# Performance work log

Hardware: AMD Instinct MI355X
Metric: run time of the kernel (lower is better)

## Reference

```python
import jax, jax.numpy as jnp
import numpy as np

N_NODES = 100000
N_GRAPHS = 64


def gcn_conv(x, src, dst, W, b, num_nodes):
    """PyG GCNConv: add self-loops, symmetric deg normalization, aggregate at dst."""
    h = x @ W  # [N, out]
    ones_e = jnp.ones(src.shape[0], dtype=x.dtype)
    # degree includes self-loop (+1)
    deg = jax.ops.segment_sum(ones_e, dst, num_segments=num_nodes) + 1.0
    dinv = jnp.where(deg > 0, 1.0 / jnp.sqrt(deg), 0.0)  # deg>=1 always here
    norm = dinv[src] * dinv[dst]  # [E]
    msg = h[src] * norm[:, None]  # gather + scale
    agg = jax.ops.segment_sum(msg, dst, num_segments=num_nodes)
    # self-loop contribution: norm_ii = dinv[i]^2
    agg = agg + h * (dinv * dinv)[:, None]
    return agg + b


def global_mean_pool(x, batch, num_graphs):
    sums = jax.ops.segment_sum(x, batch, num_segments=num_graphs)
    counts = jax.ops.segment_sum(jnp.ones(x.shape[0], dtype=x.dtype), batch,
                                 num_segments=num_graphs)
    return sums / jnp.maximum(counts, 1.0)[:, None]


def setup_inputs() -> dict:
    key = jax.random.key(0)
    ks = jax.random.split(key, 8)
    H = 128
    x = jax.random.normal(ks[0], (N_NODES, 4), dtype=jnp.float32)
    edge_index = jax.random.randint(ks[1], (2, 1600000), 0, N_NODES, dtype=jnp.int64 if jax.config.read('jax_enable_x64') else jnp.int32)
    batch = jnp.sort(jax.random.randint(ks[2], (N_NODES,), 0, N_GRAPHS))
    def glorot(k, shape):
        fan_in, fan_out = shape
        lim = np.sqrt(6.0 / (fan_in + fan_out))
        return jax.random.uniform(k, shape, jnp.float32, -lim, lim)
    return {
        'x': x,
        'edge_index': edge_index,
        'batch': batch,
        'W1': glorot(ks[3], (4, H)), 'b1': jnp.zeros((H,), jnp.float32),
        'W2': glorot(ks[4], (H, H)), 'b2': jnp.zeros((H,), jnp.float32),
        'W3': glorot(ks[5], (H, H)), 'b3': jnp.zeros((H,), jnp.float32),
        'Wl': glorot(ks[6], (H, 2)), 'bl': jnp.zeros((2,), jnp.float32),
    }


def reference(x, edge_index, batch, W1, b1, W2, b2, W3, b3, Wl, bl):
    src, dst = edge_index[0], edge_index[1]
    h = jax.nn.relu(gcn_conv(x, src, dst, W1, b1, N_NODES))
    h = jax.nn.relu(gcn_conv(h, src, dst, W2, b2, N_NODES))
    h = jax.nn.relu(gcn_conv(h, src, dst, W3, b3, N_NODES))
    g = global_mean_pool(h, batch, N_GRAPHS)  # [G, H]
    logits = g @ Wl + bl  # [G, 2]
    return jax.nn.log_softmax(logits, axis=1)
```

## Files before the change

### kernel.cpp

```cpp
#include <hip/hip_runtime.h>

#define HDIM 128
#define NGRAPH 64

#define BSHIFT 9
#define NBUCK 196
#define BCAP 48
#define BSTR 49
#define RCAP 9216
#define BIN_CHUNK 4096

typedef __attribute__((ext_vector_type(8))) short short8;
typedef __attribute__((ext_vector_type(4))) float floatx4;
typedef __attribute__((ext_vector_type(2))) float floatx2;

__device__ __forceinline__ float bf2f(unsigned short u) {
    union { unsigned int i; float f; } v;
    v.i = ((unsigned int)u) << 16;
    return v.f;
}
__device__ __forceinline__ unsigned short f2bf(float f) {
    unsigned int u = __float_as_uint(f);
    u += 0x7FFFu + ((u >> 16) & 1u);
    return (unsigned short)(u >> 16);
}

__global__ __launch_bounds__(256) void k_misc(int* __restrict__ gcur,
                                              const int* __restrict__ batch,
                                              float* __restrict__ gcnt,
                                              float* __restrict__ gsum,
                                              const float* __restrict__ W2,
                                              unsigned short* __restrict__ Wp2,
                                              const float* __restrict__ W3,
                                              unsigned short* __restrict__ Wp3,
                                              int N, int nbuck) {
    int t = threadIdx.x;
    int blk = blockIdx.x;
    if (blk == 0) {
        if (t < nbuck) gcur[t] = t * RCAP;
        for (int i = t; i < NGRAPH * 128; i += 256) gsum[i] = 0.f;
        if (t < NGRAPH) {
            int g = t;
            int lo = 0, hi = N;
            while (lo < hi) { int m = (lo + hi) >> 1; if (batch[m] < g) lo = m + 1; else hi = m; }
            int lb = lo;
            lo = 0; hi = N;
            while (lo < hi) { int m = (lo + hi) >> 1; if (batch[m] < g + 1) lo = m + 1; else hi = m; }
            gcnt[g] = (float)(lo - lb);
        }
        return;
    }
    const float* W = (blk <= 64) ? W2 : W3;
    unsigned short* Wp = (blk <= 64) ? Wp2 : Wp3;
    int idx = ((blk <= 64) ? (blk - 1) : (blk - 65)) * 256 + t;
    int j = idx & 7, l = (idx >> 3) & 63, frag = idx >> 9;
    int c = frag >> 2, ks = frag & 3;
    int k = ks * 32 + ((l >> 4) & 3) * 8 + j;
    int n = c * 16 + (l & 15);
    Wp[idx] = f2bf(W[k * 128 + n]);
}


__global__ __launch_bounds__(256) void k_binA(const int* __restrict__ src,
                                              const int* __restrict__ dst,
                                              int* __restrict__ gcur,
                                              unsigned int* __restrict__ binned, int E) {
    __shared__ unsigned int bin[NBUCK * BSTR];
    __shared__ int bcnt[NBUCK];
    __shared__ int bbase[NBUCK];
    int t = threadIdx.x;
    for (int b = t; b < NBUCK; b += 256) bcnt[b] = 0;
    __syncthreads();
    int e0 = blockIdx.x * BIN_CHUNK;
    #pragma unroll
    for (int i = 0; i < BIN_CHUNK / 1024; i++) {
        int e = e0 + i * 1024 + t * 4;
        if (e + 3 < E) {
            const int4 d4 = *(const int4*)&dst[e];
            const int4 s4 = *(const int4*)&src[e];
            int dd[4] = {d4.x, d4.y, d4.z, d4.w};
            int ss[4] = {s4.x, s4.y, s4.z, s4.w};
            #pragma unroll
            for (int k = 0; k < 4; k++) {
                int d = dd[k];
                unsigned int rec = ((unsigned int)(d & 511) << 20) | (unsigned int)ss[k];
                int b = d >> BSHIFT;
                int idx = atomicAdd(&bcnt[b], 1);
                if (idx < BCAP) bin[b * BSTR + idx] = rec;
                else { int p = atomicAdd(&gcur[b], 1); binned[p] = rec; }
            }
        } else {
            for (int k = 0; k < 4; k++) {
                int e2 = e + k;
                if (e2 < E) {
                    int d = dst[e2];
                    unsigned int rec = ((unsigned int)(d & 511) << 20) | (unsigned int)src[e2];
                    int b = d >> BSHIFT;
                    int idx = atomicAdd(&bcnt[b], 1);
                    if (idx < BCAP) bin[b * BSTR + idx] = rec;
                    else { int p = atomicAdd(&gcur[b], 1); binned[p] = rec; }
                }
            }
        }
    }
    __syncthreads();
    if (t < NBUCK) {
        int cnt = min(bcnt[t], BCAP);
        bbase[t] = atomicAdd(&gcur[t], cnt);
    }
    __syncthreads();
    int wave = t >> 6, lane = t & 63;
    for (int b = wave; b < NBUCK; b += 4) {
        int cnt = min(bcnt[b], BCAP);
        int base = bbase[b];
        if (lane < cnt) binned[base + lane] = bin[b * BSTR + lane];
    }
}

__global__ __launch_bounds__(256) void k_fillB(const int* __restrict__ gcur,
                                               const unsigned int* __restrict__ binned,
                                               int* __restrict__ P,
                                               float* __restrict__ dinv,
                                               int* __restrict__ csr, int N, int nbuck) {
    __shared__ int ps[256];
    __shared__ int cnt[512];
    __shared__ int image[RCAP];
    int b = blockIdx.x;
    int t = threadIdx.x;
    int lt = (t < nbuck) ? (gcur[t] - t * RCAP) : 0;
    ps[t] = lt;
    __syncthreads();
    for (int d = 1; d < 256; d <<= 1) {
        int o = (t >= d) ? ps[t - d] : 0;
        __syncthreads();
        ps[t] += o;
        __syncthreads();
    }
    int start = (b > 0) ? ps[b - 1] : 0;
    int len = ps[b] - start;
    __syncthreads();

    int n0 = b << BSHIFT;
    int nloc = min(n0 + 512, N) - n0;
    cnt[t] = 0; cnt[t + 256] = 0;
    __syncthreads();
    const unsigned int* rb = binned + (size_t)b * RCAP;
    for (int i = t; i < len; i += 256) atomicAdd(&cnt[rb[i] >> 20], 1);
    __syncthreads();
    int c0 = cnt[2 * t], c1 = cnt[2 * t + 1];
    int pair = c0 + c1;
    __syncthreads();
    cnt[t] = pair;
    __syncthreads();
    for (int d = 1; d < 256; d <<= 1) {
        int o = (t >= d) ? cnt[t - d] : 0;
        __syncthreads();
        cnt[t] += o;
        __syncthreads();
    }
    int excl = cnt[t] - pair;
    __syncthreads();
    if (2 * t < nloc) {
        P[n0 + 2 * t] = start + excl;
        dinv[n0 + 2 * t] = rsqrtf((float)c0 + 1.0f);
    }
    if (2 * t + 1 < nloc) {
        P[n0 + 2 * t + 1] = start + excl + c0;
        dinv[n0 + 2 * t + 1] = rsqrtf((float)c1 + 1.0f);
    }
    if (b == nbuck - 1 && t == 0) P[N] = start + len;
    cnt[2 * t] = excl;
    cnt[2 * t + 1] = excl + c0;
    __syncthreads();
    for (int i = t; i < len; i += 256) {
        unsigned int rec = rb[i];
        int pos = atomicAdd(&cnt[rec >> 20], 1);
        image[pos] = (int)(rec & 0xFFFFFu);
    }
    __syncthreads();
    for (int i = t; i < len; i += 256) csr[start + i] = image[i];
}

__global__ void k_xscale(const float4* __restrict__ x, const float* __restrict__ dinv,
                         float4* __restrict__ xs, int N) {
    int n = blockIdx.x * blockDim.x + threadIdx.x;
    if (n < N) {
        float dd = dinv[n];
        float4 v = x[n];
        xs[n] = make_float4(v.x * dd, v.y * dd, v.z * dd, v.w * dd);
    }
}

__global__ void k_aggx_csr(const int* __restrict__ P, const int* __restrict__ csr,
                           const float4* __restrict__ xs, const float* __restrict__ dinv,
                           float4* __restrict__ aggx, int N) {
    int d = blockIdx.x * blockDim.x + threadIdx.x;
    if (d >= N) return;
    int s0 = P[d], s1 = P[d + 1];
    float dd = dinv[d];
    float4 sv = xs[d];
    float4 a = make_float4(sv.x * dd, sv.y * dd, sv.z * dd, sv.w * dd);
    int i = s0;
    int pre = min(s1, (s0 + 3) & ~3);
    for (; i < pre; i++) {
        float4 v = xs[csr[i]];
        a.x += v.x; a.y += v.y; a.z += v.z; a.w += v.w;
    }
    for (; i + 8 <= s1; i += 8) {
        const int4 iA = *(const int4*)&csr[i];
        const int4 iB = *(const int4*)&csr[i + 4];
        float4 vA = xs[iA.x], vB = xs[iA.y], vC = xs[iA.z], vD = xs[iA.w];
        float4 vE = xs[iB.x], vF = xs[iB.y], vG = xs[iB.z], vH = xs[iB.w];
        a.x += vA.x + vB.x + vC.x + vD.x + vE.x + vF.x + vG.x + vH.x;
        a.y += vA.y + vB.y + vC.y + vD.y + vE.y + vF.y + vG.y + vH.y;
        a.z += vA.z + vB.z + vC.z + vD.z + vE.z + vF.z + vG.z + vH.z;
        a.w += vA.w + vB.w + vC.w + vD.w + vE.w + vF.w + vG.w + vH.w;
    }
    for (; i + 4 <= s1; i += 4) {
        const int4 ix = *(const int4*)&csr[i];
        float4 vA = xs[ix.x], vB = xs[ix.y], vC = xs[ix.z], vD = xs[ix.w];
        a.x += vA.x + vB.x + vC.x + vD.x;
        a.y += vA.y + vB.y + vC.y + vD.y;
        a.z += vA.z + vB.z + vC.z + vD.z;
        a.w += vA.w + vB.w + vC.w + vD.w;
    }
    for (; i < s1; i++) {
        float4 v = xs[csr[i]];
        a.x += v.x; a.y += v.y; a.z += v.z; a.w += v.w;
    }
    aggx[d] = make_float4(a.x * dd, a.y * dd, a.z * dd, a.w * dd);
}

#define LXS 136
__global__ __launch_bounds__(256) void k_l1t2(const float4* __restrict__ aggx,
                                              const float* __restrict__ W1,
                                              const float* __restrict__ b1,
                                              const unsigned short* __restrict__ Wp,
                                              const float* __restrict__ dinv,
                                              unsigned char* __restrict__ out8, int N) {
    __shared__ unsigned short lx[64 * LXS];
    __shared__ unsigned short lw[16384];
    __shared__ float w1s[512];
    __shared__ float b1s[128];
    __shared__ float ax[64][4];
    int t = threadIdx.x;
    int n0 = blockIdx.x * 64;

    for (int i = t; i < 512; i += 256) w1s[i] = W1[i];
    if (t < 128) b1s[t] = b1[t];
    if (t < 64) {
        float4 v = (n0 + t < N) ? aggx[n0 + t] : make_float4(0.f, 0.f, 0.f, 0.f);
        ax[t][0] = v.x; ax[t][1] = v.y; ax[t][2] = v.z; ax[t][3] = v.w;
    }
    for (int ch = t; ch < 2048; ch += 256)
        *(uint4*)&lw[ch * 8] = *(const uint4*)&Wp[ch * 8];
    __syncthreads();

    for (int i = t; i < 8192; i += 256) {
        int n = i >> 7, j = i & 127;
        float v = b1s[j] + ax[n][0] * w1s[j] + ax[n][1] * w1s[128 + j]
                         + ax[n][2] * w1s[256 + j] + ax[n][3] * w1s[384 + j];
        lx[n * LXS + j] = f2bf(fmaxf(v, 0.f));
    }
    __syncthreads();

    int w = t >> 6, lane = t & 63;
    int m0 = w * 16;
    int col = lane & 15, quad = lane >> 4;

    short8 afrag[4];
    #pragma unroll
    for (int ks = 0; ks < 4; ks++)
        afrag[ks] = *(const short8*)&lx[(m0 + col) * LXS + ks * 32 + quad * 8];

    float dv[4];
    #pragma unroll
    for (int r = 0; r < 4; r++) {
        int gn = n0 + m0 + quad * 4 + r;
        dv[r] = (gn < N) ? dinv[gn] : 0.0f;
    }

    #pragma unroll
    for (int c = 0; c < 8; c++) {
        floatx4 acc = {0.f, 0.f, 0.f, 0.f};
        #pragma unroll
        for (int ks = 0; ks < 4; ks++) {
            const short8 bfrag = *(const short8*)&lw[((c * 4 + ks) * 64 + lane) * 8];
            acc = __builtin_amdgcn_mfma_f32_16x16x32_bf16(afrag[ks], bfrag, acc, 0, 0, 0);
        }
        #pragma unroll
        for (int r = 0; r < 4; r++) {
            int gn = n0 + m0 + quad * 4 + r;
            if (gn < N) {
                float v = acc[r] * dv[r];
                out8[(size_t)gn * 128 + c * 16 + col] =
                    (unsigned char)(__builtin_amdgcn_cvt_pk_fp8_f32(v, v, 0, false) & 0xFF);
            }
        }
    }
}

__global__ __launch_bounds__(256) void k_transform_mfma(const unsigned short* __restrict__ in,
                                                        const unsigned short* __restrict__ Wp,
                                                        const float* __restrict__ dinv,
                                                        unsigned char* __restrict__ out8, int N) {
    __shared__ unsigned short lx[64 * LXS];
    __shared__ unsigned short lw[16384];
    int t = threadIdx.x;
    int n0 = blockIdx.x * 64;

    for (int ch = t; ch < 1024; ch += 256) {
        int row = ch >> 4, part = ch & 15;
        uint4 val = make_uint4(0, 0, 0, 0);
        if (n0 + row < N) val = *(const uint4*)&in[(size_t)(n0 + row) * 128 + part * 8];
        *(uint4*)&lx[row * LXS + part * 8] = val;
    }
    for (int ch = t; ch < 2048; ch += 256)
        *(uint4*)&lw[ch * 8] = *(const uint4*)&Wp[ch * 8];
    __syncthreads();

    int w = t >> 6, lane = t & 63;
    int m0 = w * 16;
    int col = lane & 15, quad = lane >> 4;

    short8 afrag[4];
    #pragma unroll
    for (int ks = 0; ks < 4; ks++)
        afrag[ks] = *(const short8*)&lx[(m0 + col) * LXS + ks * 32 + quad * 8];

    float dv[4];
    #pragma unroll
    for (int r = 0; r < 4; r++) {
        int gn = n0 + m0 + quad * 4 + r;
        dv[r] = (gn < N) ? dinv[gn] : 0.0f;
    }

    #pragma unroll
    for (int c = 0; c < 8; c++) {
        floatx4 acc = {0.f, 0.f, 0.f, 0.f};
        #pragma unroll
        for (int ks = 0; ks < 4; ks++) {
            const short8 bfrag = *(const short8*)&lw[((c * 4 + ks) * 64 + lane) * 8];
            acc = __builtin_amdgcn_mfma_f32_16x16x32_bf16(afrag[ks], bfrag, acc, 0, 0, 0);
        }
        #pragma unroll
        for (int r = 0; r < 4; r++) {
            int gn = n0 + m0 + quad * 4 + r;
            if (gn < N) {
                float v = acc[r] * dv[r];
                out8[(size_t)gn * 128 + c * 16 + col] =
                    (unsigned char)(__builtin_amdgcn_cvt_pk_fp8_f32(v, v, 0, false) & 0xFF);
            }
        }
    }
}

__device__ __forceinline__ void fp8acc(unsigned int u, float& a0, float& a1,
                                       float& a2, float& a3) {
    floatx2 lo = __builtin_amdgcn_cvt_pk_f32_fp8(u, false);
    floatx2 hi = __builtin_amdgcn_cvt_pk_f32_fp8(u, true);
    a0 += lo.x; a1 += lo.y; a2 += hi.x; a3 += hi.y;
}

__device__ __forceinline__ void gather_fp8(const int* __restrict__ csr,
                                           const unsigned int* __restrict__ hs8,
                                           int s0, int s1, int lane,
                                           float& a0, float& a1, float& a2, float& a3) {
    int i = s0;
    int pre = min(s1, (s0 + 3) & ~3);
    for (; i < pre; i++)
        fp8acc(hs8[(size_t)csr[i] * 32 + lane], a0, a1, a2, a3);
    for (; i + 8 <= s1; i += 8) {
        const int4 iA = *(const int4*)&csr[i];
        const int4 iB = *(const int4*)&csr[i + 4];
        unsigned int u0 = hs8[(size_t)iA.x * 32 + lane];
        unsigned int u1 = hs8[(size_t)iA.y * 32 + lane];
        unsigned int u2 = hs8[(size_t)iA.z * 32 + lane];
        unsigned int u3 = hs8[(size_t)iA.w * 32 + lane];
        unsigned int u4 = hs8[(size_t)iB.x * 32 + lane];
        unsigned int u5 = hs8[(size_t)iB.y * 32 + lane];
        unsigned int u6 = hs8[(size_t)iB.z * 32 + lane];
        unsigned int u7 = hs8[(size_t)iB.w * 32 + lane];
        fp8acc(u0, a0, a1, a2, a3); fp8acc(u1, a0, a1, a2, a3);
        fp8acc(u2, a0, a1, a2, a3); fp8acc(u3, a0, a1, a2, a3);
        fp8acc(u4, a0, a1, a2, a3); fp8acc(u5, a0, a1, a2, a3);
        fp8acc(u6, a0, a1, a2, a3); fp8acc(u7, a0, a1, a2, a3);
    }
    for (; i + 4 <= s1; i += 4) {
        const int4 iA = *(const int4*)&csr[i];
        unsigned int u0 = hs8[(size_t)iA.x * 32 + lane];
        unsigned int u1 = hs8[(size_t)iA.y * 32 + lane];
        unsigned int u2 = hs8[(size_t)iA.z * 32 + lane];
        unsigned int u3 = hs8[(size_t)iA.w * 32 + lane];
        fp8acc(u0, a0, a1, a2, a3); fp8acc(u1, a0, a1, a2, a3);
        fp8acc(u2, a0, a1, a2, a3); fp8acc(u3, a0, a1, a2, a3);
    }
    for (; i < s1; i++)
        fp8acc(hs8[(size_t)csr[i] * 32 + lane], a0, a1, a2, a3);
}

__global__ __launch_bounds__(256) void k_agg_csr(const int* __restrict__ P,
                                                 const int* __restrict__ csr,
                                                 const unsigned int* __restrict__ hs8,
                                                 const float* __restrict__ dinv,
                                                 const float* __restrict__ bias,
                                                 unsigned short* __restrict__ out16,
                                                 unsigned int* __restrict__ out8,
                                                 int N, int write8) {
    int g = (blockIdx.x * 256 + threadIdx.x) >> 5;
    int lane = threadIdx.x & 31;
    if (g >= N) return;
    int s0 = P[g], s1 = P[g + 1];
    unsigned int su = hs8[(size_t)g * 32 + lane];
    floatx2 slo = __builtin_amdgcn_cvt_pk_f32_fp8(su, false);
    floatx2 shi = __builtin_amdgcn_cvt_pk_f32_fp8(su, true);
    float a0 = slo.x, a1 = slo.y, a2 = shi.x, a3 = shi.y;
    gather_fp8(csr, hs8, s0, s1, lane, a0, a1, a2, a3);
    float dd = dinv[g];
    const float4 bb = *(const float4*)&bias[lane * 4];
    float o0 = fmaxf(a0 * dd + bb.x, 0.f);
    float o1 = fmaxf(a1 * dd + bb.y, 0.f);
    float o2 = fmaxf(a2 * dd + bb.z, 0.f);
    float o3 = fmaxf(a3 * dd + bb.w, 0.f);
    if (write8) {
        unsigned int wv = __builtin_amdgcn_cvt_pk_fp8_f32(o0, o1, 0, false);
        wv = __builtin_amdgcn_cvt_pk_fp8_f32(o2, o3, wv, true);
        out8[(size_t)g * 32 + lane] = wv;
    } else {
        ushort4 o;
        o.x = f2bf(o0); o.y = f2bf(o1); o.z = f2bf(o2); o.w = f2bf(o3);
        *(ushort4*)&out16[(size_t)g * 128 + lane * 4] = o;
    }
}

#define POOL_ROWS 64
__global__ __launch_bounds__(128) void k_pool8(const unsigned char* __restrict__ h8,
                                               const int* __restrict__ batch,
                                               float* __restrict__ gsum, int N) {
    int n0 = blockIdx.x * POOL_ROWS;
    if (n0 >= N) return;
    int len = min(POOL_ROWS, N - n0);
    int j = threadIdx.x;
    int bFirst = batch[n0];
    int bLast = batch[n0 + len - 1];
    if (bFirst == bLast) {
        float acc = 0.f;
        #pragma unroll 8
        for (int i = 0; i < len; i++) {
            unsigned int u = h8[(size_t)(n0 + i) * 128 + j];
            floatx2 lo = __builtin_amdgcn_cvt_pk_f32_fp8(u, false);
            acc += lo.x;
        }
        unsafeAtomicAdd(&gsum[(size_t)bFirst * 128 + j], acc);
    } else {
        float acc = 0.f;
        int cur = bFirst;
        for (int i = 0; i < len; i++) {
            int b = batch[n0 + i];
            if (b != cur) {
                unsafeAtomicAdd(&gsum[(size_t)cur * 128 + j], acc);
                acc = 0.f; cur = b;
            }
            unsigned int u = h8[(size_t)(n0 + i) * 128 + j];
            floatx2 lo = __builtin_amdgcn_cvt_pk_f32_fp8(u, false);
            acc += lo.x;
        }
        unsafeAtomicAdd(&gsum[(size_t)cur * 128 + j], acc);
    }
}

__global__ __launch_bounds__(256) void k_head(const float* __restrict__ gsum,
                                              const float* __restrict__ gcnt,
                                              const float* __restrict__ Wl,
                                              const float* __restrict__ bl,
                                              float* __restrict__ out, int G) {
    int t = threadIdx.x;
    int g = t >> 2, q = t & 3;
    if (g >= G) return;
    float l0 = 0.f, l1 = 0.f;
    #pragma unroll
    for (int k = 0; k < 32; k++) {
        int jj = q * 32 + k;
        float v = gsum[(size_t)g * 128 + jj];
        l0 += v * Wl[jj * 2 + 0];
        l1 += v * Wl[jj * 2 + 1];
    }
    l0 += __shfl_xor(l0, 1, 64); l1 += __shfl_xor(l1, 1, 64);
    l0 += __shfl_xor(l0, 2, 64); l1 += __shfl_xor(l1, 2, 64);
    if (q == 0) {
        float inv = 1.0f / fmaxf(gcnt[g], 1.0f);
        l0 = l0 * inv + bl[0];
        l1 = l1 * inv + bl[1];
        float m = fmaxf(l0, l1);
        float lse = m + logf(expf(l0 - m) + expf(l1 - m));
        out[g * 2 + 0] = l0 - lse;
        out[g * 2 + 1] = l1 - lse;
    }
}


extern "C" void kernel_launch(void* const* d_in, const int* in_sizes, int n_in,
                              void* d_out, int out_size, void* d_ws, size_t ws_size,
                              hipStream_t stream) {
    const float* x   = (const float*)d_in[0];
    const int*   ei  = (const int*)d_in[1];
    const int*   bat = (const int*)d_in[2];
    const float* W1  = (const float*)d_in[3];
    const float* b1  = (const float*)d_in[4];
    const float* W2  = (const float*)d_in[5];
    const float* b2  = (const float*)d_in[6];
    const float* W3  = (const float*)d_in[7];
    const float* b3  = (const float*)d_in[8];
    const float* Wl  = (const float*)d_in[9];
    const float* bl  = (const float*)d_in[10];

    const int N = in_sizes[0] / 4;
    const int E = in_sizes[1] / 2;
    const int* srcI = ei;
    const int* dstI = ei + E;

    const int nbuck = (N + 511) >> BSHIFT;
    const int pAlloc = ((N + 1 + 3) & ~3) + 4;

    float* wsf  = (float*)d_ws;
    float* dinv = wsf;
    int*   P    = (int*)(dinv + N);
    int*   csr  = P + pAlloc;
    float* aggx = (float*)(csr + E);
    unsigned short* bufA16 = (unsigned short*)(aggx + (size_t)N * 4);
    unsigned char*  hs8    = (unsigned char*)(bufA16 + (size_t)N * 128);
    unsigned short* Wp2    = (unsigned short*)(hs8 + (size_t)N * 128);
    unsigned short* Wp3    = Wp2 + 16384;
    float* gsum = (float*)(Wp3 + 16384);
    float* gcnt = gsum + NGRAPH * 128;
    int*   gcur = (int*)(gcnt + NGRAPH);
    unsigned int* binned = (unsigned int*)hs8;
    float* xs4 = (float*)bufA16;
    unsigned char* h3f8  = (unsigned char*)bufA16;

    k_misc<<<129, 256, 0, stream>>>(gcur, bat, gcnt, gsum, W2, Wp2, W3, Wp3, N, nbuck);
    k_binA<<<(E + BIN_CHUNK - 1) / BIN_CHUNK, 256, 0, stream>>>(srcI, dstI, gcur, binned, E);
    k_fillB<<<nbuck, 256, 0, stream>>>(gcur, binned, P, dinv, csr, N, nbuck);

    k_xscale<<<(N + 255) / 256, 256, 0, stream>>>((const float4*)x, dinv, (float4*)xs4, N);
    k_aggx_csr<<<(N + 255) / 256, 256, 0, stream>>>(P, csr, (const float4*)xs4, dinv,
                                                    (float4*)aggx, N);
    k_l1t2<<<(N + 63) / 64, 256, 0, stream>>>((const float4*)aggx, W1, b1, Wp2, dinv, hs8, N);

    k_agg_csr<<<(N * 32 + 255) / 256, 256, 0, stream>>>(P, csr, (const unsigned int*)hs8,
                                                        dinv, b2, bufA16, nullptr, N, 0);

    k_transform_mfma<<<(N + 63) / 64, 256, 0, stream>>>(bufA16, Wp3, dinv, hs8, N);
    k_agg_csr<<<(N * 32 + 255) / 256, 256, 0, stream>>>(P, csr, (const unsigned int*)hs8,
                                                        dinv, b3, nullptr,
                                                        (unsigned int*)h3f8, N, 1);

    k_pool8<<<(N + POOL_ROWS - 1) / POOL_ROWS, 128, 0, stream>>>(h3f8, bat, gsum, N);
    k_head<<<1, 256, 0, stream>>>(gsum, gcnt, Wl, bl, (float*)d_out, NGRAPH);
}
```

Baseline: 320.9 us.

## Fuse x scaling into CSR fill, split edge gather per node, fuse pooling

Folds the dinv scaling of x into k_fillB and drops the separate k_xscale launch. Aggregation now gives each node a full 64-lane wave, with two 32-lane halves each gathering half the edge range and combining through a cross-half shuffle. The final-layer aggregation writes its ReLU output straight into per-graph sums through shared memory and atomics, which removes the fp8 intermediate store and the k_pool8 pass. The cost is twice as many threads per node, half of them idle in the epilogue, plus a block-wide sync in the pooling path. Pooling now uses full fp32 outputs instead of fp8-rounded ones.

New measurement: 375.7 us. +17.1%, slower.

```diff
diff --git a/kernel.cpp b/kernel.cpp
--- a/kernel.cpp
+++ b/kernel.cpp
@@ -121,7 +121,10 @@
                                                const unsigned int* __restrict__ binned,
                                                int* __restrict__ P,
                                                float* __restrict__ dinv,
-                                               int* __restrict__ csr, int N, int nbuck) {
+                                               int* __restrict__ csr,
+                                               const float4* __restrict__ x4,
+                                               float4* __restrict__ xs4,
+                                               int N, int nbuck) {
     __shared__ int ps[256];
     __shared__ int cnt[512];
     __shared__ int image[RCAP];
@@ -161,12 +164,20 @@
     int excl = cnt[t] - pair;
     __syncthreads();
     if (2 * t < nloc) {
-        P[n0 + 2 * t] = start + excl;
-        dinv[n0 + 2 * t] = rsqrtf((float)c0 + 1.0f);
+        int n = n0 + 2 * t;
+        float dv0 = rsqrtf((float)c0 + 1.0f);
+        P[n] = start + excl;
+        dinv[n] = dv0;
+        float4 xv = x4[n];
+        xs4[n] = make_float4(xv.x * dv0, xv.y * dv0, xv.z * dv0, xv.w * dv0);
     }
     if (2 * t + 1 < nloc) {
-        P[n0 + 2 * t + 1] = start + excl + c0;
-        dinv[n0 + 2 * t + 1] = rsqrtf((float)c1 + 1.0f);
+        int n = n0 + 2 * t + 1;
+        float dv1 = rsqrtf((float)c1 + 1.0f);
+        P[n] = start + excl + c0;
+        dinv[n] = dv1;
+        float4 xv = x4[n];
+        xs4[n] = make_float4(xv.x * dv1, xv.y * dv1, xv.z * dv1, xv.w * dv1);
     }
     if (b == nbuck - 1 && t == 0) P[N] = start + len;
     cnt[2 * t] = excl;
@@ -179,16 +190,6 @@
     }
     __syncthreads();
     for (int i = t; i < len; i += 256) csr[start + i] = image[i];
-}
-
-__global__ void k_xscale(const float4* __restrict__ x, const float* __restrict__ dinv,
-                         float4* __restrict__ xs, int N) {
-    int n = blockIdx.x * blockDim.x + threadIdx.x;
-    if (n < N) {
-        float dd = dinv[n];
-        float4 v = x[n];
-        xs[n] = make_float4(v.x * dd, v.y * dd, v.z * dd, v.w * dd);
-    }
 }
 
 __global__ void k_aggx_csr(const int* __restrict__ P, const int* __restrict__ csr,
@@ -405,67 +406,68 @@
                                                  const float* __restrict__ dinv,
                                                  const float* __restrict__ bias,
                                                  unsigned short* __restrict__ out16,
-                                                 unsigned int* __restrict__ out8,
-                                                 int N, int write8) {
-    int g = (blockIdx.x * 256 + threadIdx.x) >> 5;
-    int lane = threadIdx.x & 31;
-    if (g >= N) return;
-    int s0 = P[g], s1 = P[g + 1];
-    unsigned int su = hs8[(size_t)g * 32 + lane];
-    floatx2 slo = __builtin_amdgcn_cvt_pk_f32_fp8(su, false);
-    floatx2 shi = __builtin_amdgcn_cvt_pk_f32_fp8(su, true);
-    float a0 = slo.x, a1 = slo.y, a2 = shi.x, a3 = shi.y;
-    gather_fp8(csr, hs8, s0, s1, lane, a0, a1, a2, a3);
-    float dd = dinv[g];
-    const float4 bb = *(const float4*)&bias[lane * 4];
-    float o0 = fmaxf(a0 * dd + bb.x, 0.f);
-    float o1 = fmaxf(a1 * dd + bb.y, 0.f);
-    float o2 = fmaxf(a2 * dd + bb.z, 0.f);
-    float o3 = fmaxf(a3 * dd + bb.w, 0.f);
-    if (write8) {
-        unsigned int wv = __builtin_amdgcn_cvt_pk_fp8_f32(o0, o1, 0, false);
-        wv = __builtin_amdgcn_cvt_pk_fp8_f32(o2, o3, wv, true);
-        out8[(size_t)g * 32 + lane] = wv;
+                                                 const int* __restrict__ batch,
+                                                 float* __restrict__ gsum,
+                                                 int N, int mode) {
+    __shared__ float psum[4][128];
+    int wv = threadIdx.x >> 6;
+    int g = blockIdx.x * 4 + wv;
+    int lane = threadIdx.x & 63;
+    int half = lane >> 5;
+    int fl = lane & 31;
+
+    float a0 = 0.f, a1 = 0.f, a2 = 0.f, a3 = 0.f;
+    int s0 = 0, s1 = 0;
+    if (g < N) { s0 = P[g]; s1 = P[g + 1]; }
+    if (g < N && half == 0) {
+        unsigned int su = hs8[(size_t)g * 32 + fl];
+        fp8acc(su, a0, a1, a2, a3);
+    }
+    int mid = (s0 + s1) >> 1;
+    int lo = half ? mid : s0;
+    int hi = half ? s1 : mid;
+    gather_fp8(csr, hs8, lo, hi, fl, a0, a1, a2, a3);
+
+    a0 += __shfl_xor(a0, 32);
+    a1 += __shfl_xor(a1, 32);
+    a2 += __shfl_xor(a2, 32);
+    a3 += __shfl_xor(a3, 32);
+
+    float o0 = 0.f, o1 = 0.f, o2 = 0.f, o3 = 0.f;
+    if (g < N && half == 0) {
+        float dd = dinv[g];
+        const float4 bb = *(const float4*)&bias[fl * 4];
+        o0 = fmaxf(a0 * dd + bb.x, 0.f);
+        o1 = fmaxf(a1 * dd + bb.y, 0.f);
+        o2 = fmaxf(a2 * dd + bb.z, 0.f);
+        o3 = fmaxf(a3 * dd + bb.w, 0.f);
+    }
+
+    if (mode == 0) {
+        if (g < N && half == 0) {
+            ushort4 o;
+            o.x = f2bf(o0); o.y = f2bf(o1); o.z = f2bf(o2); o.w = f2bf(o3);
+            *(ushort4*)&out16[(size_t)g * 128 + fl * 4] = o;
+        }
     } else {
-        ushort4 o;
-        o.x = f2bf(o0); o.y = f2bf(o1); o.z = f2bf(o2); o.w = f2bf(o3);
-        *(ushort4*)&out16[(size_t)g * 128 + lane * 4] = o;
-    }
-}
-
-#define POOL_ROWS 64
-__global__ __launch_bounds__(128) void k_pool8(const unsigned char* __restrict__ h8,
-                                               const int* __restrict__ batch,
-                                               float* __restrict__ gsum, int N) {
-    int n0 = blockIdx.x * POOL_ROWS;
-    if (n0 >= N) return;
-    int len = min(POOL_ROWS, N - n0);
-    int j = threadIdx.x;
-    int bFirst = batch[n0];
-    int bLast = batch[n0 + len - 1];
-    if (bFirst == bLast) {
-        float acc = 0.f;
-        #pragma unroll 8
-        for (int i = 0; i < len; i++) {
-            unsigned int u = h8[(size_t)(n0 + i) * 128 + j];
-            floatx2 lo = __builtin_amdgcn_cvt_pk_f32_fp8(u, false);
-            acc += lo.x;
-        }
-        unsafeAtomicAdd(&gsum[(size_t)bFirst * 128 + j], acc);
-    } else {
-        float acc = 0.f;
-        int cur = bFirst;
-        for (int i = 0; i < len; i++) {
-            int b = batch[n0 + i];
-            if (b != cur) {
-                unsafeAtomicAdd(&gsum[(size_t)cur * 128 + j], acc);
-                acc = 0.f; cur = b;
+        if (half == 0)
+            *(float4*)&psum[wv][fl * 4] = make_float4(o0, o1, o2, o3);
+        __syncthreads();
+        int t = threadIdx.x;
+        if (t < 128) {
+            int gb0 = blockIdx.x * 4;
+            int glast = min(gb0 + 3, N - 1);
+            int b0 = batch[gb0], b3 = batch[glast];
+            if (b0 == b3 && gb0 + 3 < N) {
+                float s = psum[0][t] + psum[1][t] + psum[2][t] + psum[3][t];
+                unsafeAtomicAdd(&gsum[(size_t)b0 * 128 + t], s);
+            } else {
+                #pragma unroll
+                for (int r = 0; r < 4; r++)
+                    if (gb0 + r < N)
+                        unsafeAtomicAdd(&gsum[(size_t)batch[gb0 + r] * 128 + t], psum[r][t]);
             }
-            unsigned int u = h8[(size_t)(n0 + i) * 128 + j];
-            floatx2 lo = __builtin_amdgcn_cvt_pk_f32_fp8(u, false);
-            acc += lo.x;
-        }
-        unsafeAtomicAdd(&gsum[(size_t)cur * 128 + j], acc);
+        }
     }
 }
 
@@ -536,25 +538,22 @@
     int*   gcur = (int*)(gcnt + NGRAPH);
     unsigned int* binned = (unsigned int*)hs8;
     float* xs4 = (float*)bufA16;
-    unsigned char* h3f8  = (unsigned char*)bufA16;
 
     k_misc<<<129, 256, 0, stream>>>(gcur, bat, gcnt, gsum, W2, Wp2, W3, Wp3, N, nbuck);
     k_binA<<<(E + BIN_CHUNK - 1) / BIN_CHUNK, 256, 0, stream>>>(srcI, dstI, gcur, binned, E);
-    k_fillB<<<nbuck, 256, 0, stream>>>(gcur, binned, P, dinv, csr, N, nbuck);
-
-    k_xscale<<<(N + 255) / 256, 256, 0, stream>>>((const float4*)x, dinv, (float4*)xs4, N);
+    k_fillB<<<nbuck, 256, 0, stream>>>(gcur, binned, P, dinv, csr,
+                                       (const float4*)x, (float4*)xs4, N, nbuck);
+
     k_aggx_csr<<<(N + 255) / 256, 256, 0, stream>>>(P, csr, (const float4*)xs4, dinv,
                                                     (float4*)aggx, N);
     k_l1t2<<<(N + 63) / 64, 256, 0, stream>>>((const float4*)aggx, W1, b1, Wp2, dinv, hs8, N);
 
-    k_agg_csr<<<(N * 32 + 255) / 256, 256, 0, stream>>>(P, csr, (const unsigned int*)hs8,
-                                                        dinv, b2, bufA16, nullptr, N, 0);
+    k_agg_csr<<<(N + 3) / 4, 256, 0, stream>>>(P, csr, (const unsigned int*)hs8,
+                                               dinv, b2, bufA16, nullptr, nullptr, N, 0);
 
     k_transform_mfma<<<(N + 63) / 64, 256, 0, stream>>>(bufA16, Wp3, dinv, hs8, N);
-    k_agg_csr<<<(N * 32 + 255) / 256, 256, 0, stream>>>(P, csr, (const unsigned int*)hs8,
-                                                        dinv, b3, nullptr,
-                                                        (unsigned int*)h3f8, N, 1);
-
-    k_pool8<<<(N + POOL_ROWS - 1) / POOL_ROWS, 128, 0, stream>>>(h3f8, bat, gsum, N);
+    k_agg_csr<<<(N + 3) / 4, 256, 0, stream>>>(P, csr, (const unsigned int*)hs8,
+                                               dinv, b3, nullptr, bat, gsum, N, 1);
+
     k_head<<<1, 256, 0, stream>>>(gsum, gcnt, Wl, bl, (float*)d_out, NGRAPH);
 }
```
